# Performance work log

Hardware: AMD Instinct MI355X
Metric: run time of the kernel (lower is better)

## Reference

```python
import jax, jax.numpy as jnp
import numpy as np

H, DI, N, K, R, FF = 2048, 4096, 16, 4, 128, 5632
B, S = 2, 1024
EPS = 1e-6


def rmsnorm(x, w):
    v = jnp.mean(x * x, axis=-1, keepdims=True)
    return x * jax.lax.rsqrt(v + EPS) * w


def setup_inputs() -> dict:
    key = jax.random.key(0)
    ks = jax.random.split(key, 16)
    sc = 0.02
    inp = {
        "hidden_states": jax.random.normal(ks[0], (B, S, H), jnp.float32),
        "input_ln_w": jnp.ones((H,), jnp.float32),
        "w_in": jax.random.normal(ks[1], (2 * DI, H), jnp.float32) * sc,
        "conv_w": jax.random.normal(ks[2], (DI, 1, K), jnp.float32) * 0.3,
        "conv_b": jax.random.normal(ks[3], (DI,), jnp.float32) * sc,
        "w_x": jax.random.normal(ks[4], (R + 2 * N, DI), jnp.float32) * sc,
        "dt_ln_w": jnp.ones((R,), jnp.float32),
        "b_ln_w": jnp.ones((N,), jnp.float32),
        "c_ln_w": jnp.ones((N,), jnp.float32),
        "w_dt": jax.random.normal(ks[5], (DI, R), jnp.float32) * sc,
        "b_dt": jax.random.normal(ks[6], (DI,), jnp.float32) * sc - 4.0,
        "A_log": jnp.broadcast_to(jnp.log(jnp.arange(1, N + 1, dtype=jnp.float32)), (DI, N)),
        "D_skip": jnp.ones((DI,), jnp.float32),
        "w_out": jax.random.normal(ks[7], (H, DI), jnp.float32) * sc,
        "pre_ff_ln_w": jnp.ones((H,), jnp.float32),
        "w_gate": jax.random.normal(ks[8], (FF, H), jnp.float32) * sc,
        "w_up": jax.random.normal(ks[9], (FF, H), jnp.float32) * sc,
        "w_down": jax.random.normal(ks[10], (H, FF), jnp.float32) * sc,
    }
    return inp


def causal_conv1d(x, w, b):
    # x: [B,S,DI], w: [DI,1,K] depthwise, left-pad K-1 (causal)
    y = jax.lax.conv_general_dilated(
        x.transpose(0, 2, 1), w,
        window_strides=(1,), padding=[(K - 1, 0)],
        dimension_numbers=("NCH", "OIH", "NCH"),
        feature_group_count=DI)
    return (y + b[None, :, None]).transpose(0, 2, 1)


def selective_scan(u, A, Bm, Cm, Dp, dt):
    # u,dt: [B,S,DI]; A: [DI,N]; Bm,Cm: [B,S,N]
    def step(h, xs):
        dt_t, B_t, C_t, u_t = xs  # [B,DI],[B,N],[B,N],[B,DI]
        dA = jnp.exp(dt_t[:, :, None] * A)                      # [B,DI,N]
        dBu = dt_t[:, :, None] * B_t[:, None, :] * u_t[:, :, None]
        h = dA * h + dBu
        y = jnp.einsum("bdn,bn->bd", h, C_t)
        return h, y

    xs = (dt.transpose(1, 0, 2), Bm.transpose(1, 0, 2),
          Cm.transpose(1, 0, 2), u.transpose(1, 0, 2))
    h0 = jnp.zeros((u.shape[0], DI, N), u.dtype)
    _, ys = jax.lax.scan(step, h0, xs)
    return ys.transpose(1, 0, 2) + u * Dp  # [B,S,DI]


def reference(hidden_states, input_ln_w, w_in, conv_w, conv_b, w_x, dt_ln_w,
              b_ln_w, c_ln_w, w_dt, b_dt, A_log, D_skip, w_out, pre_ff_ln_w,
              w_gate, w_up, w_down):
    residual = hidden_states
    x = rmsnorm(hidden_states, input_ln_w)

    # --- Mamba mixer ---
    proj = x @ w_in.T                       # [B,S,2*DI]
    u, gate = jnp.split(proj, 2, axis=-1)
    u = jax.nn.silu(causal_conv1d(u, conv_w, conv_b))
    ssm_p = u @ w_x.T                       # [B,S,R+2N]
    t_r, Bm, Cm = jnp.split(ssm_p, [R, R + N], axis=-1)
    t_r = rmsnorm(t_r, dt_ln_w)
    Bm = rmsnorm(Bm, b_ln_w)
    Cm = rmsnorm(Cm, c_ln_w)
    dt = jax.nn.softplus(t_r @ w_dt.T + b_dt)  # [B,S,DI]
    A = -jnp.exp(A_log)
    y = selective_scan(u, A, Bm, Cm, D_skip, dt)
    y = y * jax.nn.silu(gate)
    mixer_out = y @ w_out.T                  # [B,S,H]

    hidden = residual + mixer_out
    residual = hidden
    h = rmsnorm(hidden, pre_ff_ln_w)
    ff = (jax.nn.silu(h @ w_gate.T) * (h @ w_up.T)) @ w_down.T
    return residual + ff
```

## Files before the change

kernel.cpp:

```cpp
#include <hip/hip_runtime.h>
#include <stdint.h>

#define H_   2048
#define DI_  4096
#define N_   16
#define K_   4
#define R_   128
#define FF_  5632
#define B_   2
#define S_   1024
#define MROWS (B_*S_)
#define PCH  32
#define CSTEPS (S_/PCH)

typedef float f32x4 __attribute__((ext_vector_type(4)));
typedef float f32x2 __attribute__((ext_vector_type(2)));
typedef __bf16 bf16x8 __attribute__((ext_vector_type(8)));

#define LOG2E 1.4426950408889634f
#define LN2   0.6931471805599453f

__device__ __forceinline__ unsigned short f2bf(float f) {
    union { float f; unsigned u; } v; v.f = f;
    unsigned r = v.u + 0x7fffu + ((v.u >> 16) & 1u);
    return (unsigned short)(r >> 16);
}

__device__ __forceinline__ float bf2f(unsigned short u) {
    union { unsigned u; float f; } v; v.u = ((unsigned)u) << 16;
    return v.f;
}

__device__ __forceinline__ float fexp2(float x) { return __builtin_amdgcn_exp2f(x); }
__device__ __forceinline__ float flog2(float x) { return __builtin_amdgcn_logf(x); }

__device__ __forceinline__ float softplus2(float v) {
    return (v > 20.f) ? v : LN2 * flog2(1.f + fexp2(v * LOG2E));
}

__device__ __forceinline__ void gload16(const void* g, void* lds) {
    __builtin_amdgcn_global_load_lds(
        (const __attribute__((address_space(1))) unsigned int*)(uintptr_t)g,
        (__attribute__((address_space(3))) unsigned int*)(unsigned int)(uintptr_t)lds,
        16, 0, 0);
}

__global__ __launch_bounds__(256, 2)
void gemm_bt(const unsigned short* __restrict__ A, const unsigned short* __restrict__ Bt,
             void* __restrict__ Cv, int M, int N, int K, int Kc, int obf)
{
    __shared__ __align__(16) unsigned short As[128 * 64];
    __shared__ __align__(16) unsigned short Bs[128 * 64];
    const int t = threadIdx.x;
    const int l = t & 63;
    const int wv = t >> 6;

    int nwg = gridDim.x * gridDim.y;
    int wg = blockIdx.y * gridDim.x + blockIdx.x;
    if ((nwg & 7) == 0) {
        int q = nwg >> 3;
        wg = (wg & 7) * q + (wg >> 3);
    }
    const int bx = wg / gridDim.y;
    const int by = wg % gridDim.y;
    const long m0 = (long)by * 128;
    const long n0 = (long)bx * 128;
    const int wm = (wv >> 1) * 64;
    const int wn = (wv & 1) * 64;
    const long kstart = (long)blockIdx.z * Kc;
    const long cbase = (long)blockIdx.z * M * (long)N;

    f32x4 acc[4][4] = {};

    const int tr = t >> 3;
    const int cs = (t & 7) ^ (tr & 7);
    const unsigned short* gA = A + (m0 + tr) * (long)K + kstart + cs * 8;
    const unsigned short* gB = Bt + (n0 + tr) * (long)K + kstart + cs * 8;
    const unsigned ldsbase = (unsigned)(t & 192) * 16;

    for (int kt = 0; kt < Kc; kt += 64) {
#pragma unroll
        for (int j = 0; j < 4; ++j) {
            gload16(gA + (long)j * 32 * K, (char*)As + j * 4096 + ldsbase);
            gload16(gB + (long)j * 32 * K, (char*)Bs + j * 4096 + ldsbase);
        }
        gA += 64; gB += 64;
        __syncthreads();
#pragma unroll
        for (int k0 = 0; k0 < 2; ++k0) {
            bf16x8 af[4], bfr[4];
#pragma unroll
            for (int i = 0; i < 4; ++i) {
                int rowa = wm + i * 16 + (l & 15);
                int ca = (k0 * 4 + (l >> 4)) ^ (rowa & 7);
                af[i] = *(const bf16x8*)(As + rowa * 64 + ca * 8);
                int rowb = wn + i * 16 + (l & 15);
                int cb = (k0 * 4 + (l >> 4)) ^ (rowb & 7);
                bfr[i] = *(const bf16x8*)(Bs + rowb * 64 + cb * 8);
            }
#pragma unroll
            for (int i = 0; i < 4; ++i)
#pragma unroll
                for (int jn = 0; jn < 4; ++jn)
                    acc[i][jn] = __builtin_amdgcn_mfma_f32_16x16x32_bf16(
                        af[i], bfr[jn], acc[i][jn], 0, 0, 0);
        }
        __syncthreads();
    }

    const int crow = (l >> 4) * 4;
    const int ccol = l & 15;
    float* Cf = (float*)Cv + cbase;
    unsigned short* Cb = (unsigned short*)Cv + cbase;
#pragma unroll
    for (int i = 0; i < 4; ++i) {
#pragma unroll
        for (int jn = 0; jn < 4; ++jn) {
            long row = m0 + wm + i * 16 + crow;
            long col = n0 + wn + jn * 16 + ccol;
            if (obf) {
                unsigned short* cp = Cb + row * (long)N + col;
#pragma unroll
                for (int q = 0; q < 4; ++q) cp[(long)q * N] = f2bf(acc[i][jn][q]);
            } else {
                float* cp = Cf + row * (long)N + col;
#pragma unroll
                for (int q = 0; q < 4; ++q) cp[(long)q * N] = acc[i][jn][q];
            }
        }
    }
}

__global__ __launch_bounds__(512, 1)
void gemm_bt256(const unsigned short* __restrict__ A, const unsigned short* __restrict__ Bt,
                void* __restrict__ Cv, int M, int N, int K, int Kc, int obf)
{
    __shared__ __align__(16) unsigned short As[2][256 * 64];
    __shared__ __align__(16) unsigned short Bs[2][256 * 64];
    const int t = threadIdx.x;
    const int l = t & 63;
    const int wv = t >> 6;
    const int wm = wv >> 2;
    const int wn = wv & 3;

    int nwg = gridDim.x * gridDim.y;
    int wg = blockIdx.y * gridDim.x + blockIdx.x;
    if ((nwg & 7) == 0) {
        int q = nwg >> 3;
        wg = (wg & 7) * q + (wg >> 3);
    }
    const int bx = wg / gridDim.y;
    const int by = wg % gridDim.y;
    const long m0 = (long)by * 256;
    const long n0 = (long)bx * 256;
    const long kstart = (long)blockIdx.z * Kc;
    const long cbase = (long)blockIdx.z * M * (long)N;

    f32x4 acc[8][4] = {};

    const int cs = (t & 7) ^ ((t >> 3) & 7);
    const unsigned short* gA = A + (m0 + (t >> 3)) * (long)K + kstart + cs * 8;
    const unsigned short* gB = Bt + (n0 + (t >> 3)) * (long)K + kstart + cs * 8;
    const int NT = Kc >> 6;

#pragma unroll
    for (int i = 0; i < 4; ++i)
        gload16(gA + (long)i * 64 * K, &As[0][t * 8 + i * 4096]);
#pragma unroll
    for (int i = 0; i < 4; ++i)
        gload16(gB + (long)i * 64 * K, &Bs[0][t * 8 + i * 4096]);

    for (int kt = 0; kt < NT; ++kt) {
        const int buf = kt & 1;
        const long koff = (long)((kt + 1 < NT) ? (kt + 1) : kt) * 64;
#pragma unroll
        for (int i = 0; i < 4; ++i)
            gload16(gA + koff + (long)i * 64 * K, &As[buf ^ 1][t * 8 + i * 4096]);
        asm volatile("s_waitcnt vmcnt(4)" ::: "memory");
        __builtin_amdgcn_sched_barrier(0);
        __builtin_amdgcn_s_barrier();
        __builtin_amdgcn_sched_barrier(0);
        {
            bf16x8 af[8], bfr[4];
#pragma unroll
            for (int nf = 0; nf < 4; ++nf) {
                int rowb = wn * 64 + nf * 16 + (l & 15);
                int cb = (l >> 4) ^ (rowb & 7);
                bfr[nf] = *(const bf16x8*)(&Bs[buf][rowb * 64 + cb * 8]);
            }
#pragma unroll
            for (int mf = 0; mf < 8; ++mf) {
                int rowa = wm * 128 + mf * 16 + (l & 15);
                int ca = (l >> 4) ^ (rowa & 7);
                af[mf] = *(const bf16x8*)(&As[buf][rowa * 64 + ca * 8]);
            }
            __builtin_amdgcn_s_setprio(1);
#pragma unroll
            for (int mf = 0; mf < 8; ++mf)
#pragma unroll
                for (int nf = 0; nf < 4; ++nf)
                    acc[mf][nf] = __builtin_amdgcn_mfma_f32_16x16x32_bf16(
                        af[mf], bfr[nf], acc[mf][nf], 0, 0, 0);
            __builtin_amdgcn_s_setprio(0);
        }
        __builtin_amdgcn_sched_barrier(0);
#pragma unroll
        for (int i = 0; i < 4; ++i)
            gload16(gB + koff + (long)i * 64 * K, &Bs[buf ^ 1][t * 8 + i * 4096]);
        {
            bf16x8 af[8], bfr[4];
#pragma unroll
            for (int nf = 0; nf < 4; ++nf) {
                int rowb = wn * 64 + nf * 16 + (l & 15);
                int cb = (4 + (l >> 4)) ^ (rowb & 7);
                bfr[nf] = *(const bf16x8*)(&Bs[buf][rowb * 64 + cb * 8]);
            }
#pragma unroll
            for (int mf = 0; mf < 8; ++mf) {
                int rowa = wm * 128 + mf * 16 + (l & 15);
                int ca = (4 + (l >> 4)) ^ (rowa & 7);
                af[mf] = *(const bf16x8*)(&As[buf][rowa * 64 + ca * 8]);
            }
            __builtin_amdgcn_s_setprio(1);
#pragma unroll
            for (int mf = 0; mf < 8; ++mf)
#pragma unroll
                for (int nf = 0; nf < 4; ++nf)
                    acc[mf][nf] = __builtin_amdgcn_mfma_f32_16x16x32_bf16(
                        af[mf], bfr[nf], acc[mf][nf], 0, 0, 0);
            __builtin_amdgcn_s_setprio(0);
        }
        __builtin_amdgcn_sched_barrier(0);
        __builtin_amdgcn_s_barrier();
        __builtin_amdgcn_sched_barrier(0);
    }

    const int crow = (l >> 4) * 4;
    const int ccol = l & 15;
    float* Cf = (float*)Cv + cbase;
    unsigned short* Cb = (unsigned short*)Cv + cbase;
#pragma unroll
    for (int mf = 0; mf < 8; ++mf) {
#pragma unroll
        for (int nf = 0; nf < 4; ++nf) {
            long row = m0 + wm * 128 + mf * 16 + crow;
            long col = n0 + wn * 64 + nf * 16 + ccol;
            if (obf) {
                unsigned short* cp = Cb + row * (long)N + col;
#pragma unroll
                for (int q = 0; q < 4; ++q) cp[(long)q * N] = f2bf(acc[mf][nf][q]);
            } else {
                float* cp = Cf + row * (long)N + col;
#pragma unroll
                for (int q = 0; q < 4; ++q) cp[(long)q * N] = acc[mf][nf][q];
            }
        }
    }
}

__global__ __launch_bounds__(256)
void cvt_bf16(const float* __restrict__ x, unsigned short* __restrict__ y, long n)
{
    long i = ((long)blockIdx.x * 256 + threadIdx.x) * 4;
    if (i >= n) return;
    float4 v = *(const float4*)(x + i);
    ushort4 o;
    o.x = f2bf(v.x); o.y = f2bf(v.y); o.z = f2bf(v.z); o.w = f2bf(v.w);
    *(ushort4*)(y + i) = o;
}

__global__ __launch_bounds__(256)
void cvt_pad_wx(const float* __restrict__ x, unsigned short* __restrict__ y)
{
    long i = ((long)blockIdx.x * 256 + threadIdx.x) * 4;
    int row = (int)(i >> 12);
    ushort4 o;
    if (row < 160) {
        float4 v = *(const float4*)(x + i);
        o.x = f2bf(v.x); o.y = f2bf(v.y); o.z = f2bf(v.z); o.w = f2bf(v.w);
    } else { o.x = 0; o.y = 0; o.z = 0; o.w = 0; }
    *(ushort4*)(y + i) = o;
}

__global__ __launch_bounds__(256)
void rmsnorm_cast(const float* __restrict__ x, const float* __restrict__ w,
                  unsigned short* __restrict__ out)
{
    const long row = blockIdx.x;
    const float* xr = x + row * H_ + threadIdx.x * 8;
    float4 v0 = *(const float4*)xr;
    float4 v1 = *(const float4*)(xr + 4);
    float xv[8] = {v0.x, v0.y, v0.z, v0.w, v1.x, v1.y, v1.z, v1.w};
    float s = 0.f;
#pragma unroll
    for (int j = 0; j < 8; ++j) s += xv[j] * xv[j];
#pragma unroll
    for (int m = 32; m; m >>= 1) s += __shfl_xor(s, m);
    __shared__ float red[4];
    if ((threadIdx.x & 63) == 0) red[threadIdx.x >> 6] = s;
    __syncthreads();
    s = red[0] + red[1] + red[2] + red[3];
    float inv = rsqrtf(s * (1.f / H_) + 1e-6f);
    const float* wr = w + threadIdx.x * 8;
    unsigned short* op = out + row * H_ + threadIdx.x * 8;
    ushort4 o0, o1;
    o0.x = f2bf(xv[0] * inv * wr[0]); o0.y = f2bf(xv[1] * inv * wr[1]);
    o0.z = f2bf(xv[2] * inv * wr[2]); o0.w = f2bf(xv[3] * inv * wr[3]);
    o1.x = f2bf(xv[4] * inv * wr[4]); o1.y = f2bf(xv[5] * inv * wr[5]);
    o1.z = f2bf(xv[6] * inv * wr[6]); o1.w = f2bf(xv[7] * inv * wr[7]);
    *(ushort4*)op = o0;
    *(ushort4*)(op + 4) = o1;
}

__global__ __launch_bounds__(256)
void add_rmsnorm(const float* __restrict__ a, const unsigned short* __restrict__ mx,
                 const float* __restrict__ w, float* __restrict__ hid,
                 unsigned short* __restrict__ hb)
{
    const long row = blockIdx.x;
    const long off = row * H_ + threadIdx.x * 8;
    float xv[8];
    {
        float4 a0 = *(const float4*)(a + off);
        float4 a1 = *(const float4*)(a + off + 4);
        xv[0] = a0.x; xv[1] = a0.y; xv[2] = a0.z; xv[3] = a0.w;
        xv[4] = a1.x; xv[5] = a1.y; xv[6] = a1.z; xv[7] = a1.w;
    }
#pragma unroll
    for (int z = 0; z < 4; ++z) {
        const unsigned short* mz = mx + (long)z * MROWS * H_ + off;
        ushort4 b0 = *(const ushort4*)mz;
        ushort4 b1 = *(const ushort4*)(mz + 4);
        xv[0] += bf2f(b0.x); xv[1] += bf2f(b0.y); xv[2] += bf2f(b0.z); xv[3] += bf2f(b0.w);
        xv[4] += bf2f(b1.x); xv[5] += bf2f(b1.y); xv[6] += bf2f(b1.z); xv[7] += bf2f(b1.w);
    }
    float s = 0.f;
#pragma unroll
    for (int j = 0; j < 8; ++j) s += xv[j] * xv[j];
#pragma unroll
    for (int m = 32; m; m >>= 1) s += __shfl_xor(s, m);
    __shared__ float red[4];
    if ((threadIdx.x & 63) == 0) red[threadIdx.x >> 6] = s;
    __syncthreads();
    s = red[0] + red[1] + red[2] + red[3];
    float inv = rsqrtf(s * (1.f / H_) + 1e-6f);
    float4 h0, h1;
    h0.x = xv[0]; h0.y = xv[1]; h0.z = xv[2]; h0.w = xv[3];
    h1.x = xv[4]; h1.y = xv[5]; h1.z = xv[6]; h1.w = xv[7];
    *(float4*)(hid + off) = h0;
    *(float4*)(hid + off + 4) = h1;
    const float* wr = w + threadIdx.x * 8;
    ushort4 o0, o1;
    o0.x = f2bf(xv[0] * inv * wr[0]); o0.y = f2bf(xv[1] * inv * wr[1]);
    o0.z = f2bf(xv[2] * inv * wr[2]); o0.w = f2bf(xv[3] * inv * wr[3]);
    o1.x = f2bf(xv[4] * inv * wr[4]); o1.y = f2bf(xv[5] * inv * wr[5]);
    o1.z = f2bf(xv[6] * inv * wr[6]); o1.w = f2bf(xv[7] * inv * wr[7]);
    *(ushort4*)(hb + off) = o0;
    *(ushort4*)(hb + off + 4) = o1;
}

__global__ __launch_bounds__(256)
void conv_silu(const unsigned short* __restrict__ proj, const float* __restrict__ cw,
               const float* __restrict__ cb, unsigned short* __restrict__ ub)
{
    long i = (long)blockIdx.x * 256 + threadIdx.x;
    int d = (int)(i & (DI_ - 1));
    long sd = i >> 12;
    int s = (int)(sd & (S_ - 1));
    long rb = sd * (2 * DI_) + d;
    float w0 = cw[d * 4], w1 = cw[d * 4 + 1], w2 = cw[d * 4 + 2], w3 = cw[d * 4 + 3];
    float acc = cb[d] + w3 * bf2f(proj[rb]);
    if (s >= 1) acc += w2 * bf2f(proj[rb - 2 * DI_]);
    if (s >= 2) acc += w1 * bf2f(proj[rb - 4 * DI_]);
    if (s >= 3) acc += w0 * bf2f(proj[rb - 6 * DI_]);
    float r = acc / (1.f + __expf(-acc));
    ub[i] = f2bf(r);
}

__global__ __launch_bounds__(256)
void ssm_norms(const float* __restrict__ ssmp, const float* __restrict__ wdt,
               const float* __restrict__ wb, const float* __restrict__ wc,
               unsigned short* __restrict__ trb, float* __restrict__ Bm,
               float* __restrict__ Cm)
{
    const long row = (long)blockIdx.x * 4 + (threadIdx.x >> 6);
    const int l = threadIdx.x & 63;
    float x0 = 0.f, x1 = 0.f, xb = 0.f, xc = 0.f;
#pragma unroll
    for (int z = 0; z < 8; ++z) {
        const float* rp = ssmp + (long)z * (MROWS * 256) + row * 256;
        x0 += rp[l];
        x1 += rp[64 + l];
        xb += rp[128 + (l & 15)];
        xc += rp[144 + (l & 15)];
    }
    float s = x0 * x0 + x1 * x1;
#pragma unroll
    for (int m = 32; m; m >>= 1) s += __shfl_xor(s, m);
    float inv = rsqrtf(s * (1.f / R_) + 1e-6f);
    trb[row * R_ + l] = f2bf(x0 * inv * wdt[l]);
    trb[row * R_ + 64 + l] = f2bf(x1 * inv * wdt[64 + l]);

    float sb = xb * xb, sc = xc * xc;
#pragma unroll
    for (int m = 8; m; m >>= 1) { sb += __shfl_xor(sb, m); sc += __shfl_xor(sc, m); }
    float invb = rsqrtf(sb * (1.f / N_) + 1e-6f);
    float invc = rsqrtf(sc * (1.f / N_) + 1e-6f);
    if (l < 16) {
        Bm[row * N_ + l] = xb * invb * wb[l];
        Cm[row * N_ + l] = xc * invc * wc[l];
    }
}


__global__ __launch_bounds__(256)
void scan_partA(const unsigned short* __restrict__ ub, const unsigned short* __restrict__ dtraw,
                const float* __restrict__ bdt, const float* __restrict__ Bm,
                const float* __restrict__ A_log,
                float* __restrict__ TRH, float* __restrict__ TRS)
{
    const int w = __builtin_amdgcn_readfirstlane(threadIdx.x >> 6);
    const int l = threadIdx.x & 63;
    const int task = blockIdx.x * 4 + w;
    const int dchunk = task >> 5;
    const int p = task & 31;
    const int gch0 = dchunk * 64;
    const int batch = gch0 >> 12;
    const int d0 = gch0 & (DI_ - 1);
    const int d = d0 + l;
    const long bS = (long)batch * S_;
    const int t0 = p * CSTEPS;

    float Av2[16];
#pragma unroll
    for (int n = 0; n < 16; ++n)
        Av2[n] = -fexp2(A_log[(long)d * N_ + n] * LOG2E) * LOG2E;
    const float bias = bdt[d];

    float h[16];
#pragma unroll
    for (int n = 0; n < 16; ++n) h[n] = 0.f;
    float sdt = 0.f;

    float uN = bf2f(ub[(bS + t0) * DI_ + d]);
    float tN = bf2f(dtraw[(bS + t0) * DI_ + d]);
    float BN[16];
    {
        const float* Bp = Bm + (bS + t0) * N_;
#pragma unroll
        for (int n = 0; n < 16; ++n) BN[n] = Bp[n];
    }

    for (int s = 0; s < CSTEPS; ++s) {
        float uC = uN, tC = tN;
        float BC[16];
#pragma unroll
        for (int n = 0; n < 16; ++n) BC[n] = BN[n];
        if (s + 1 < CSTEPS) {
            long r2 = bS + t0 + s + 1;
            uN = bf2f(ub[r2 * DI_ + d]);
            tN = bf2f(dtraw[r2 * DI_ + d]);
            const float* Bp = Bm + r2 * N_;
#pragma unroll
            for (int n = 0; n < 16; ++n) BN[n] = Bp[n];
        }
        float dt = softplus2(tC + bias);
        float dtu = dt * uC;
        sdt += dt;
#pragma unroll
        for (int n = 0; n < 16; ++n) {
            float e = fexp2(dt * Av2[n]);
            h[n] = fmaf(e, h[n], dtu * BC[n]);
        }
    }
    float* hp = &TRH[(long)(gch0 + l) * (PCH * 16) + p * 16];
#pragma unroll
    for (int n = 0; n < 16; ++n) hp[n] = h[n];
    TRS[(long)(gch0 + l) * PCH + p] = sdt;
}

__global__ __launch_bounds__(256)
void scan_combine(const float* __restrict__ A_log, const float* __restrict__ TRS,
                  float* __restrict__ TRH)
{
    const int tid = blockIdx.x * 256 + threadIdx.x;
    const int gch = tid >> 4, n = tid & 15;
    const int d = gch & (DI_ - 1);
    const float Av = -__expf(A_log[(long)d * N_ + n]);
    const float* sp = TRS + (long)gch * PCH;
    float* hp = TRH + (long)gch * (PCH * 16) + n;
    float h = 0.f;
#pragma unroll
    for (int p = 0; p < PCH; ++p) {
        float hl = hp[p * 16];
        float e = __expf(Av * sp[p]);
        hp[p * 16] = h;
        h = hl + e * h;
    }
}

__global__ __launch_bounds__(256)
void scan_partC(const unsigned short* __restrict__ ub, const unsigned short* __restrict__ dtraw,
                const float* __restrict__ bdt, const float* __restrict__ Bm,
                const float* __restrict__ Cm, const float* __restrict__ A_log,
                const float* __restrict__ Dskip, const unsigned short* __restrict__ proj,
                const float* __restrict__ TRH, unsigned short* __restrict__ yb)
{
    const int w = __builtin_amdgcn_readfirstlane(threadIdx.x >> 6);
    const int l = threadIdx.x & 63;
    const int task = blockIdx.x * 4 + w;
    const int dchunk = task >> 5;
    const int p = task & 31;
    const int gch0 = dchunk * 64;
    const int batch = gch0 >> 12;
    const int d0 = gch0 & (DI_ - 1);
    const int d = d0 + l;
    const long bS = (long)batch * S_;
    const int t0 = p * CSTEPS;

    float Av2[16];
#pragma unroll
    for (int n = 0; n < 16; ++n)
        Av2[n] = -fexp2(A_log[(long)d * N_ + n] * LOG2E) * LOG2E;
    const float bias = bdt[d];
    const float Dv = Dskip[d];

    float h[16];
    {
        const float* hp = &TRH[(long)(gch0 + l) * (PCH * 16) + p * 16];
#pragma unroll
        for (int n = 0; n < 16; ++n) h[n] = hp[n];
    }

    float uN = bf2f(ub[(bS + t0) * DI_ + d]);
    float tN = bf2f(dtraw[(bS + t0) * DI_ + d]);
    float gN = bf2f(proj[(bS + t0) * (2L * DI_) + DI_ + d]);
    float BN[16], CN[16];
    {
        const float* Bp = Bm + (bS + t0) * N_;
        const float* Cp = Cm + (bS + t0) * N_;
#pragma unroll
        for (int n = 0; n < 16; ++n) { BN[n] = Bp[n]; CN[n] = Cp[n]; }
    }

    for (int s = 0; s < CSTEPS; ++s) {
        float uC = uN, tC = tN, gC = gN;
        float BC[16], CC_[16];
#pragma unroll
        for (int n = 0; n < 16; ++n) { BC[n] = BN[n]; CC_[n] = CN[n]; }
        if (s + 1 < CSTEPS) {
            long r2 = bS + t0 + s + 1;
            uN = bf2f(ub[r2 * DI_ + d]);
            tN = bf2f(dtraw[r2 * DI_ + d]);
            gN = bf2f(proj[r2 * (2L * DI_) + DI_ + d]);
            const float* Bp = Bm + r2 * N_;
            const float* Cp = Cm + r2 * N_;
#pragma unroll
            for (int n = 0; n < 16; ++n) { BN[n] = Bp[n]; CN[n] = Cp[n]; }
        }
        float dt = softplus2(tC + bias);
        float dtu = dt * uC;
        float y = uC * Dv;
#pragma unroll
        for (int n = 0; n < 16; ++n) {
            float e = fexp2(dt * Av2[n]);
            h[n] = fmaf(e, h[n], dtu * BC[n]);
            y = fmaf(h[n], CC_[n], y);
        }
        float eg = fexp2(-gC * LOG2E);
        float sl = gC * __builtin_amdgcn_rcpf(1.f + eg);
        yb[(bS + t0 + s) * DI_ + d] = f2bf(y * sl);
    }
}

__global__ __launch_bounds__(256)
void silu_mul(const unsigned short* __restrict__ g, const unsigned short* __restrict__ u,
              unsigned short* __restrict__ out, long n)
{
    long i = ((long)blockIdx.x * 256 + threadIdx.x) * 4;
    if (i >= n) return;
    ushort4 gv = *(const ushort4*)(g + i);
    ushort4 uv = *(const ushort4*)(u + i);
    float g0 = bf2f(gv.x), g1 = bf2f(gv.y), g2 = bf2f(gv.z), g3 = bf2f(gv.w);
    ushort4 o;
    o.x = f2bf(g0 / (1.f + __expf(-g0)) * bf2f(uv.x));
    o.y = f2bf(g1 / (1.f + __expf(-g1)) * bf2f(uv.y));
    o.z = f2bf(g2 / (1.f + __expf(-g2)) * bf2f(uv.z));
    o.w = f2bf(g3 / (1.f + __expf(-g3)) * bf2f(uv.w));
    *(ushort4*)(out + i) = o;
}

__global__ __launch_bounds__(256)
void final_add(const float* __restrict__ a, const unsigned short* __restrict__ b,
               float* __restrict__ y, long n)
{
    long i = ((long)blockIdx.x * 256 + threadIdx.x) * 4;
    if (i >= n) return;
    float4 av = *(const float4*)(a + i);
    float4 o = av;
#pragma unroll
    for (int z = 0; z < 4; ++z) {
        ushort4 bv = *(const ushort4*)(b + (long)z * MROWS * H_ + i);
        o.x += bf2f(bv.x); o.y += bf2f(bv.y); o.z += bf2f(bv.z); o.w += bf2f(bv.w);
    }
    *(float4*)(y + i) = o;
}

extern "C" void kernel_launch(void* const* d_in, const int* in_sizes, int n_in,
                              void* d_out, int out_size, void* d_ws, size_t ws_size,
                              hipStream_t stream)
{
    const float* hs     = (const float*)d_in[0];
    const float* ln_in  = (const float*)d_in[1];
    const float* w_in   = (const float*)d_in[2];
    const float* conv_w = (const float*)d_in[3];
    const float* conv_b = (const float*)d_in[4];
    const float* w_x    = (const float*)d_in[5];
    const float* dt_ln  = (const float*)d_in[6];
    const float* b_ln   = (const float*)d_in[7];
    const float* c_ln   = (const float*)d_in[8];
    const float* w_dt   = (const float*)d_in[9];
    const float* b_dt   = (const float*)d_in[10];
    const float* A_log  = (const float*)d_in[11];
    const float* Dskip  = (const float*)d_in[12];
    const float* w_out  = (const float*)d_in[13];
    const float* ln_ff  = (const float*)d_in[14];
    const float* w_gate = (const float*)d_in[15];
    const float* w_up   = (const float*)d_in[16];
    const float* w_down = (const float*)d_in[17];
    float* out = (float*)d_out;
    char* ws = (char*)d_ws;

    unsigned short* WB    = (unsigned short*)(ws + 0L);
    unsigned short* XB    = (unsigned short*)(ws + 33554432L);
    unsigned short* PROJ  = (unsigned short*)(ws + 41943040L);
    unsigned short* MIX   = (unsigned short*)(ws + 41943040L);
    unsigned short* GF    = (unsigned short*)(ws + 41943040L);
    unsigned short* FFT   = (unsigned short*)(ws + 41943040L);
    unsigned short* FFACT = (unsigned short*)(ws + 109051904L);
    unsigned short* UB    = (unsigned short*)(ws + 142606336L);
    float*          HID   = (float*)(ws + 142606336L);
    unsigned short* TRB   = (unsigned short*)(ws + 159383552L);
    float*          BM    = (float*)(ws + 159907840L);
    float*          CM    = (float*)(ws + 160038912L);
    float*          TRS   = (float*)(ws + 160169984L);
    float*          SSMP  = (float*)(ws + 161218560L);
    unsigned short* DTRAW = (unsigned short*)(ws + 161218560L);
    unsigned short* UPF   = (unsigned short*)(ws + 161218560L);
    float*          TRH   = (float*)(ws + 194772992L);
    unsigned short* YB    = (unsigned short*)(ws + 227803136L);
    unsigned short* HB    = XB;

    auto gemm = [&](const unsigned short* A, const unsigned short* Bt, void* C,
                    int M, int N, int K, int kch, int obf) {
        dim3 g(N / 128, M / 128, kch);
        gemm_bt<<<g, 256, 0, stream>>>(A, Bt, C, M, N, K, K / kch, obf);
    };
    auto gemm256 = [&](const unsigned short* A, const unsigned short* Bt, void* C,
                       int M, int N, int K, int kch, int obf) {
        dim3 g(N / 256, M / 256, kch);
        gemm_bt256<<<g, 512, 0, stream>>>(A, Bt, C, M, N, K, K / kch, obf);
    };
    auto cvt = [&](const float* x, unsigned short* y, long n) {
        cvt_bf16<<<(int)((n / 4 + 255) / 256), 256, 0, stream>>>(x, y, n);
    };

    cvt(w_in, WB, (long)2 * DI_ * H_);
    rmsnorm_cast<<<MROWS, 256, 0, stream>>>(hs, ln_in, XB);
    gemm256(XB, WB, PROJ, MROWS, 2 * DI_, H_, 1, 1);
    conv_silu<<<(MROWS * DI_) / 256, 256, 0, stream>>>(PROJ, conv_w, conv_b, UB);
    cvt_pad_wx<<<(256 * DI_ / 4) / 256, 256, 0, stream>>>(w_x, WB);
    gemm(UB, WB, SSMP, MROWS, 256, DI_, 8, 0);
    ssm_norms<<<MROWS / 4, 256, 0, stream>>>(SSMP, dt_ln, b_ln, c_ln, TRB, BM, CM);
    cvt(w_dt, WB, (long)DI_ * R_);
    gemm(TRB, WB, DTRAW, MROWS, DI_, R_, 1, 1);
    scan_partA<<<(B_ * DI_ / 64) * PCH / 4, 256, 0, stream>>>(UB, DTRAW, b_dt, BM,
                                                              A_log, TRH, TRS);
    scan_combine<<<(B_ * DI_ * N_) / 256, 256, 0, stream>>>(A_log, TRS, TRH);
    scan_partC<<<(B_ * DI_ / 64) * PCH / 4, 256, 0, stream>>>(UB, DTRAW, b_dt, BM, CM,
                                                              A_log, Dskip, PROJ, TRH, YB);
    cvt(w_out, WB, (long)H_ * DI_);
    gemm256(YB, WB, MIX, MROWS, H_, DI_, 4, 1);
    add_rmsnorm<<<MROWS, 256, 0, stream>>>(hs, MIX, ln_ff, HID, HB);
    cvt(w_gate, WB, (long)FF_ * H_);
    gemm256(HB, WB, GF, MROWS, FF_, H_, 1, 1);
    cvt(w_up, WB, (long)FF_ * H_);
    gemm256(HB, WB, UPF, MROWS, FF_, H_, 1, 1);
    silu_mul<<<(int)(((long)MROWS * FF_ / 4 + 255) / 256), 256, 0, stream>>>(
        GF, UPF, FFACT, (long)MROWS * FF_);
    cvt(w_down, WB, (long)H_ * FF_);
    gemm256(FFACT, WB, FFT, MROWS, H_, FF_, 4, 1);
    final_add<<<(int)(((long)MROWS * H_ / 4 + 255) / 256), 256, 0, stream>>>(
        HID, FFT, out, (long)MROWS * H_);
}
```

Before: 508.2 us.

## Fuse fp32-to-bf16 weight conversion into the 256-tile GEMM B-operand loads

Removes the separate cvt_bf16 passes over w_in, w_out, w_gate, w_up and w_down. The 256x256 GEMM now reads the fp32 weights directly into registers, converts them to bf16 in-kernel and stores them into swizzled LDS after the second MFMA half. The A operand still uses direct-to-LDS loads, and the wait counts are adjusted to match. This saves a full read-write pass over the weights per call. In exchange, each M tile re-reads twice as many B bytes from global memory, and the loop gains VALU conversion work and register pressure.

```diff
diff --git a/kernel.cpp b/kernel.cpp
--- a/kernel.cpp
+++ b/kernel.cpp
@@ -132,7 +132,7 @@
 }
 
 __global__ __launch_bounds__(512, 1)
-void gemm_bt256(const unsigned short* __restrict__ A, const unsigned short* __restrict__ Bt,
+void gemm_bt256(const unsigned short* __restrict__ A, const float* __restrict__ Btf,
                 void* __restrict__ Cv, int M, int N, int K, int Kc, int obf)
 {
     __shared__ __align__(16) unsigned short As[2][256 * 64];
@@ -160,23 +160,47 @@
 
     const int cs = (t & 7) ^ ((t >> 3) & 7);
     const unsigned short* gA = A + (m0 + (t >> 3)) * (long)K + kstart + cs * 8;
-    const unsigned short* gB = Bt + (n0 + (t >> 3)) * (long)K + kstart + cs * 8;
+    const float* gB = Btf + (n0 + (t >> 3)) * (long)K + kstart + cs * 8;
     const int NT = Kc >> 6;
 
+    {
+        float4 p0[4], p1[4];
+#pragma unroll
+        for (int i = 0; i < 4; ++i) {
+            const float* p = gB + (long)i * 64 * K;
+            p0[i] = *(const float4*)p;
+            p1[i] = *(const float4*)(p + 4);
+        }
+#pragma unroll
+        for (int i = 0; i < 4; ++i) {
+            union { unsigned short us[8]; f32x4 v; } pk;
+            pk.us[0] = f2bf(p0[i].x); pk.us[1] = f2bf(p0[i].y);
+            pk.us[2] = f2bf(p0[i].z); pk.us[3] = f2bf(p0[i].w);
+            pk.us[4] = f2bf(p1[i].x); pk.us[5] = f2bf(p1[i].y);
+            pk.us[6] = f2bf(p1[i].z); pk.us[7] = f2bf(p1[i].w);
+            *(f32x4*)(&Bs[0][t * 8 + i * 4096]) = pk.v;
+        }
+        asm volatile("s_waitcnt lgkmcnt(0)" ::: "memory");
+    }
 #pragma unroll
     for (int i = 0; i < 4; ++i)
         gload16(gA + (long)i * 64 * K, &As[0][t * 8 + i * 4096]);
-#pragma unroll
-    for (int i = 0; i < 4; ++i)
-        gload16(gB + (long)i * 64 * K, &Bs[0][t * 8 + i * 4096]);
 
     for (int kt = 0; kt < NT; ++kt) {
         const int buf = kt & 1;
         const long koff = (long)((kt + 1 < NT) ? (kt + 1) : kt) * 64;
+        float4 p0[4], p1[4];
+#pragma unroll
+        for (int i = 0; i < 4; ++i) {
+            const float* p = gB + koff + (long)i * 64 * K;
+            p0[i] = *(const float4*)p;
+            p1[i] = *(const float4*)(p + 4);
+        }
+        __builtin_amdgcn_sched_barrier(0);
 #pragma unroll
         for (int i = 0; i < 4; ++i)
             gload16(gA + koff + (long)i * 64 * K, &As[buf ^ 1][t * 8 + i * 4096]);
-        asm volatile("s_waitcnt vmcnt(4)" ::: "memory");
+        asm volatile("s_waitcnt vmcnt(12)" ::: "memory");
         __builtin_amdgcn_sched_barrier(0);
         __builtin_amdgcn_s_barrier();
         __builtin_amdgcn_sched_barrier(0);
@@ -204,9 +228,6 @@
             __builtin_amdgcn_s_setprio(0);
         }
         __builtin_amdgcn_sched_barrier(0);
-#pragma unroll
-        for (int i = 0; i < 4; ++i)
-            gload16(gB + koff + (long)i * 64 * K, &Bs[buf ^ 1][t * 8 + i * 4096]);
         {
             bf16x8 af[8], bfr[4];
 #pragma unroll
@@ -230,6 +251,17 @@
                         af[mf], bfr[nf], acc[mf][nf], 0, 0, 0);
             __builtin_amdgcn_s_setprio(0);
         }
+        __builtin_amdgcn_sched_barrier(0);
+#pragma unroll
+        for (int i = 0; i < 4; ++i) {
+            union { unsigned short us[8]; f32x4 v; } pk;
+            pk.us[0] = f2bf(p0[i].x); pk.us[1] = f2bf(p0[i].y);
+            pk.us[2] = f2bf(p0[i].z); pk.us[3] = f2bf(p0[i].w);
+            pk.us[4] = f2bf(p1[i].x); pk.us[5] = f2bf(p1[i].y);
+            pk.us[6] = f2bf(p1[i].z); pk.us[7] = f2bf(p1[i].w);
+            *(f32x4*)(&Bs[buf ^ 1][t * 8 + i * 4096]) = pk.v;
+        }
+        asm volatile("s_waitcnt lgkmcnt(0)" ::: "memory");
         __builtin_amdgcn_sched_barrier(0);
         __builtin_amdgcn_s_barrier();
         __builtin_amdgcn_sched_barrier(0);
@@ -656,18 +688,17 @@
         dim3 g(N / 128, M / 128, kch);
         gemm_bt<<<g, 256, 0, stream>>>(A, Bt, C, M, N, K, K / kch, obf);
     };
-    auto gemm256 = [&](const unsigned short* A, const unsigned short* Bt, void* C,
+    auto gemm256 = [&](const unsigned short* A, const float* Btf, void* C,
                        int M, int N, int K, int kch, int obf) {
         dim3 g(N / 256, M / 256, kch);
-        gemm_bt256<<<g, 512, 0, stream>>>(A, Bt, C, M, N, K, K / kch, obf);
+        gemm_bt256<<<g, 512, 0, stream>>>(A, Btf, C, M, N, K, K / kch, obf);
     };
     auto cvt = [&](const float* x, unsigned short* y, long n) {
         cvt_bf16<<<(int)((n / 4 + 255) / 256), 256, 0, stream>>>(x, y, n);
     };
 
-    cvt(w_in, WB, (long)2 * DI_ * H_);
     rmsnorm_cast<<<MROWS, 256, 0, stream>>>(hs, ln_in, XB);
-    gemm256(XB, WB, PROJ, MROWS, 2 * DI_, H_, 1, 1);
+    gemm256(XB, w_in, PROJ, MROWS, 2 * DI_, H_, 1, 1);
     conv_silu<<<(MROWS * DI_) / 256, 256, 0, stream>>>(PROJ, conv_w, conv_b, UB);
     cvt_pad_wx<<<(256 * DI_ / 4) / 256, 256, 0, stream>>>(w_x, WB);
     gemm(UB, WB, SSMP, MROWS, 256, DI_, 8, 0);
@@ -679,17 +710,13 @@
     scan_combine<<<(B_ * DI_ * N_) / 256, 256, 0, stream>>>(A_log, TRS, TRH);
     scan_partC<<<(B_ * DI_ / 64) * PCH / 4, 256, 0, stream>>>(UB, DTRAW, b_dt, BM, CM,
                                                               A_log, Dskip, PROJ, TRH, YB);
-    cvt(w_out, WB, (long)H_ * DI_);
-    gemm256(YB, WB, MIX, MROWS, H_, DI_, 4, 1);
+    gemm256(YB, w_out, MIX, MROWS, H_, DI_, 4, 1);
     add_rmsnorm<<<MROWS, 256, 0, stream>>>(hs, MIX, ln_ff, HID, HB);
-    cvt(w_gate, WB, (long)FF_ * H_);
-    gemm256(HB, WB, GF, MROWS, FF_, H_, 1, 1);
-    cvt(w_up, WB, (long)FF_ * H_);
-    gemm256(HB, WB, UPF, MROWS, FF_, H_, 1, 1);
+    gemm256(HB, w_gate, GF, MROWS, FF_, H_, 1, 1);
+    gemm256(HB, w_up, UPF, MROWS, FF_, H_, 1, 1);
     silu_mul<<<(int)(((long)MROWS * FF_ / 4 + 255) / 256), 256, 0, stream>>>(
         GF, UPF, FFACT, (long)MROWS * FF_);
-    cvt(w_down, WB, (long)H_ * FF_);
-    gemm256(FFACT, WB, FFT, MROWS, H_, FF_, 4, 1);
+    gemm256(FFACT, w_down, FFT, MROWS, H_, FF_, 4, 1);
     final_add<<<(int)(((long)MROWS * H_ / 4 + 255) / 256), 256, 0, stream>>>(
         HID, FFT, out, (long)MROWS * H_);
 }
```

After: 614.4 us. 20.9% more time.

## Merge gate/up GEMMs into one split-K launch and vectorize conv_silu

Applied to the files above, without the earlier changes.

The gate and up weights are converted into one contiguous buffer so a single GEMM with N=2*FF and a split-K of 2 replaces two separate GEMMs. The activation kernel then sums the two bf16 partial outputs for gate and up before applying SiLU and the multiply. Separately, conv_silu now processes four channels per thread with vector loads. Split-K writes twice as much intermediate bf16 data and rounds each partial sum to bf16, which costs some accuracy. Workspace buffers are remapped to make room for the merged output.

```diff
diff --git a/kernel.cpp b/kernel.cpp
--- a/kernel.cpp
+++ b/kernel.cpp
@@ -363,18 +363,35 @@
 void conv_silu(const unsigned short* __restrict__ proj, const float* __restrict__ cw,
                const float* __restrict__ cb, unsigned short* __restrict__ ub)
 {
-    long i = (long)blockIdx.x * 256 + threadIdx.x;
+    long i = ((long)blockIdx.x * 256 + threadIdx.x) * 4;
     int d = (int)(i & (DI_ - 1));
     long sd = i >> 12;
     int s = (int)(sd & (S_ - 1));
     long rb = sd * (2 * DI_) + d;
-    float w0 = cw[d * 4], w1 = cw[d * 4 + 1], w2 = cw[d * 4 + 2], w3 = cw[d * 4 + 3];
-    float acc = cb[d] + w3 * bf2f(proj[rb]);
-    if (s >= 1) acc += w2 * bf2f(proj[rb - 2 * DI_]);
-    if (s >= 2) acc += w1 * bf2f(proj[rb - 4 * DI_]);
-    if (s >= 3) acc += w0 * bf2f(proj[rb - 6 * DI_]);
-    float r = acc / (1.f + __expf(-acc));
-    ub[i] = f2bf(r);
+    ushort4 x0 = *(const ushort4*)(proj + rb);
+    ushort4 x1 = {0, 0, 0, 0}, x2 = {0, 0, 0, 0}, x3 = {0, 0, 0, 0};
+    if (s >= 1) x1 = *(const ushort4*)(proj + rb - 2 * DI_);
+    if (s >= 2) x2 = *(const ushort4*)(proj + rb - 4 * DI_);
+    if (s >= 3) x3 = *(const ushort4*)(proj + rb - 6 * DI_);
+    float4 bias = *(const float4*)(cb + d);
+    unsigned short xs0[4] = {x0.x, x0.y, x0.z, x0.w};
+    unsigned short xs1[4] = {x1.x, x1.y, x1.z, x1.w};
+    unsigned short xs2[4] = {x2.x, x2.y, x2.z, x2.w};
+    unsigned short xs3[4] = {x3.x, x3.y, x3.z, x3.w};
+    float bs[4] = {bias.x, bias.y, bias.z, bias.w};
+    unsigned short os[4];
+#pragma unroll
+    for (int j = 0; j < 4; ++j) {
+        float4 wj = *(const float4*)(cw + (d + j) * 4);
+        float acc = bs[j] + wj.w * bf2f(xs0[j]);
+        if (s >= 1) acc += wj.z * bf2f(xs1[j]);
+        if (s >= 2) acc += wj.y * bf2f(xs2[j]);
+        if (s >= 3) acc += wj.x * bf2f(xs3[j]);
+        float r = acc / (1.f + __expf(-acc));
+        os[j] = f2bf(r);
+    }
+    ushort4 o; o.x = os[0]; o.y = os[1]; o.z = os[2]; o.w = os[3];
+    *(ushort4*)(ub + i) = o;
 }
 
 __global__ __launch_bounds__(256)
@@ -574,19 +591,29 @@
 }
 
 __global__ __launch_bounds__(256)
-void silu_mul(const unsigned short* __restrict__ g, const unsigned short* __restrict__ u,
-              unsigned short* __restrict__ out, long n)
+void silu_mul2(const unsigned short* __restrict__ gfu, unsigned short* __restrict__ out,
+               long n)
 {
     long i = ((long)blockIdx.x * 256 + threadIdx.x) * 4;
     if (i >= n) return;
-    ushort4 gv = *(const ushort4*)(g + i);
-    ushort4 uv = *(const ushort4*)(u + i);
-    float g0 = bf2f(gv.x), g1 = bf2f(gv.y), g2 = bf2f(gv.z), g3 = bf2f(gv.w);
-    ushort4 o;
-    o.x = f2bf(g0 / (1.f + __expf(-g0)) * bf2f(uv.x));
-    o.y = f2bf(g1 / (1.f + __expf(-g1)) * bf2f(uv.y));
-    o.z = f2bf(g2 / (1.f + __expf(-g2)) * bf2f(uv.z));
-    o.w = f2bf(g3 / (1.f + __expf(-g3)) * bf2f(uv.w));
+    long m = i / FF_;
+    int f = (int)(i - m * FF_);
+    const long NW = 2L * FF_;
+    const unsigned short* r0 = gfu + m * NW;
+    const unsigned short* r1 = gfu + (long)MROWS * NW + m * NW;
+    ushort4 g0 = *(const ushort4*)(r0 + f);
+    ushort4 g1 = *(const ushort4*)(r1 + f);
+    ushort4 u0 = *(const ushort4*)(r0 + FF_ + f);
+    ushort4 u1 = *(const ushort4*)(r1 + FF_ + f);
+    float gv[4] = {bf2f(g0.x) + bf2f(g1.x), bf2f(g0.y) + bf2f(g1.y),
+                   bf2f(g0.z) + bf2f(g1.z), bf2f(g0.w) + bf2f(g1.w)};
+    float uv[4] = {bf2f(u0.x) + bf2f(u1.x), bf2f(u0.y) + bf2f(u1.y),
+                   bf2f(u0.z) + bf2f(u1.z), bf2f(u0.w) + bf2f(u1.w)};
+    unsigned short os[4];
+#pragma unroll
+    for (int j = 0; j < 4; ++j)
+        os[j] = f2bf(gv[j] / (1.f + __expf(-gv[j])) * uv[j]);
+    ushort4 o; o.x = os[0]; o.y = os[1]; o.z = os[2]; o.w = os[3];
     *(ushort4*)(out + i) = o;
 }
 
@@ -632,12 +659,12 @@
     char* ws = (char*)d_ws;
 
     unsigned short* WB    = (unsigned short*)(ws + 0L);
+    unsigned short* FFACT = (unsigned short*)(ws + 0L);
     unsigned short* XB    = (unsigned short*)(ws + 33554432L);
     unsigned short* PROJ  = (unsigned short*)(ws + 41943040L);
     unsigned short* MIX   = (unsigned short*)(ws + 41943040L);
-    unsigned short* GF    = (unsigned short*)(ws + 41943040L);
+    unsigned short* GFU   = (unsigned short*)(ws + 41943040L);
     unsigned short* FFT   = (unsigned short*)(ws + 41943040L);
-    unsigned short* FFACT = (unsigned short*)(ws + 109051904L);
     unsigned short* UB    = (unsigned short*)(ws + 142606336L);
     float*          HID   = (float*)(ws + 142606336L);
     unsigned short* TRB   = (unsigned short*)(ws + 159383552L);
@@ -646,10 +673,11 @@
     float*          TRS   = (float*)(ws + 160169984L);
     float*          SSMP  = (float*)(ws + 161218560L);
     unsigned short* DTRAW = (unsigned short*)(ws + 161218560L);
-    unsigned short* UPF   = (unsigned short*)(ws + 161218560L);
     float*          TRH   = (float*)(ws + 194772992L);
+    unsigned short* WGU   = (unsigned short*)(ws + 194772992L);
     unsigned short* YB    = (unsigned short*)(ws + 227803136L);
     unsigned short* HB    = XB;
+    FFACT = (unsigned short*)(ws + 161218560L);
 
     auto gemm = [&](const unsigned short* A, const unsigned short* Bt, void* C,
                     int M, int N, int K, int kch, int obf) {
@@ -668,7 +696,7 @@
     cvt(w_in, WB, (long)2 * DI_ * H_);
     rmsnorm_cast<<<MROWS, 256, 0, stream>>>(hs, ln_in, XB);
     gemm256(XB, WB, PROJ, MROWS, 2 * DI_, H_, 1, 1);
-    conv_silu<<<(MROWS * DI_) / 256, 256, 0, stream>>>(PROJ, conv_w, conv_b, UB);
+    conv_silu<<<(MROWS * DI_ / 4) / 256, 256, 0, stream>>>(PROJ, conv_w, conv_b, UB);
     cvt_pad_wx<<<(256 * DI_ / 4) / 256, 256, 0, stream>>>(w_x, WB);
     gemm(UB, WB, SSMP, MROWS, 256, DI_, 8, 0);
     ssm_norms<<<MROWS / 4, 256, 0, stream>>>(SSMP, dt_ln, b_ln, c_ln, TRB, BM, CM);
@@ -682,12 +710,11 @@
     cvt(w_out, WB, (long)H_ * DI_);
     gemm256(YB, WB, MIX, MROWS, H_, DI_, 4, 1);
     add_rmsnorm<<<MROWS, 256, 0, stream>>>(hs, MIX, ln_ff, HID, HB);
-    cvt(w_gate, WB, (long)FF_ * H_);
-    gemm256(HB, WB, GF, MROWS, FF_, H_, 1, 1);
-    cvt(w_up, WB, (long)FF_ * H_);
-    gemm256(HB, WB, UPF, MROWS, FF_, H_, 1, 1);
-    silu_mul<<<(int)(((long)MROWS * FF_ / 4 + 255) / 256), 256, 0, stream>>>(
-        GF, UPF, FFACT, (long)MROWS * FF_);
+    cvt(w_gate, WGU, (long)FF_ * H_);
+    cvt(w_up, WGU + (long)FF_ * H_, (long)FF_ * H_);
+    gemm256(HB, WGU, GFU, MROWS, 2 * FF_, H_, 2, 1);
+    silu_mul2<<<(int)(((long)MROWS * FF_ / 4 + 255) / 256), 256, 0, stream>>>(
+        GFU, FFACT, (long)MROWS * FF_);
     cvt(w_down, WB, (long)H_ * FF_);
     gemm256(FFACT, WB, FFT, MROWS, H_, FF_, 4, 1);
     final_add<<<(int)(((long)MROWS * H_ / 4 + 255) / 256), 256, 0, stream>>>(
```

Result: faster. 483.6 us (-4.8%).
